# Kernel optimization log

Hardware: AMD Instinct MI355X
Metric: run time of the kernel (lower is better)

## Reference

```python
import jax, jax.numpy as jnp
import numpy as np

N_NODES = 50000


def gcn_layer(x, W, b, src, dst, norm):
    # x: [N, Fin] -> [N, Fout]; PyG GCNConv: x' = D^-1/2 (A+I) D^-1/2 (x W) + b
    h = x @ W
    msg = h[src] * norm[:, None]              # gather + scale per edge (incl. self loops)
    out = jax.ops.segment_sum(msg, dst, num_segments=N_NODES)
    return out + b


def setup_inputs() -> dict:
    key = jax.random.key(0)
    ks = jax.random.split(key, 12)
    F_in, F_hid, T, E = 128, 128, 10, 1600000
    features = jax.random.normal(ks[0], (N_NODES, F_in), dtype=jnp.float32)
    edges = jax.random.randint(ks[1], (2, E), 0, N_NODES, dtype=jnp.int64)
    s = 1.0 / np.sqrt(F_in)
    W0 = jax.random.uniform(ks[2], (F_in, F_hid), jnp.float32, -s, s)
    b0 = jnp.zeros((F_hid,), jnp.float32)
    W1 = jax.random.uniform(ks[3], (F_hid, F_hid), jnp.float32, -s, s)
    b1 = jnp.zeros((F_hid,), jnp.float32)
    W2 = jax.random.uniform(ks[4], (F_hid, F_hid), jnp.float32, -s, s)
    b2 = jnp.zeros((F_hid,), jnp.float32)
    Wout = jax.random.uniform(ks[5], (F_hid, T), jnp.float32, -s, s)
    bout = jax.random.uniform(ks[6], (T,), jnp.float32, -s, s)
    return {"features": features, "edges": edges, "W0": W0, "b0": b0,
            "W1": W1, "b1": b1, "W2": W2, "b2": b2, "Wout": Wout, "bout": bout}


def reference(features, edges, W0, b0, W1, b1, W2, b2, Wout, bout):
    # Add self loops once; edge structure shared across layers.
    loop = jnp.arange(N_NODES, dtype=edges.dtype)
    src = jnp.concatenate([edges[0], loop])
    dst = jnp.concatenate([edges[1], loop])
    deg = jax.ops.segment_sum(jnp.ones_like(dst, dtype=features.dtype), dst,
                              num_segments=N_NODES)
    dinv = jnp.where(deg > 0, jax.lax.rsqrt(deg), 0.0)
    norm = dinv[src] * dinv[dst]              # [E + N]

    x = gcn_layer(features, W0, b0, src, dst, norm)
    x = gcn_layer(x, W1, b1, src, dst, norm)
    x = gcn_layer(x, W2, b2, src, dst, norm)

    pooled = jnp.mean(x, axis=0)              # [F_hid]
    logits = pooled @ Wout + bout             # [T]
    return jax.nn.log_softmax(logits, axis=0).reshape(1, -1)
```

## Files before the change

kernel.cpp:

```cpp
#include <hip/hip_runtime.h>


#define FDIM 128
#define HSZ 12500
#define NBG 64
#define BSZ 196
#define NBKT 256
#define SCB 256
#define STG 6400


__global__ void __launch_bounds__(1024)
k1_count_deg(const int* __restrict__ edges, int E, int e4, int N,
             int* __restrict__ blockCnt, int* __restrict__ partial) {
  __shared__ int h[HSZ];
  __shared__ int cnt[NBKT];
  const int t = threadIdx.x;
  const int bid = blockIdx.x;
  const int g = bid >> 6, j = bid & (NBG - 1);
  const int lo = g * HSZ;
  const int hi = min(N, lo + HSZ);
  const int hs = hi - lo;
  for (int i = t; i < hs; i += 1024) h[i] = 0;
  if (t < NBKT) cnt[t] = 0;
  __syncthreads();

  const int per4 = (e4 + SCB - 1) / SCB;
  const int i0 = bid * per4;
  const int i1 = min(e4, i0 + per4);
  const int4* s4 = (const int4*)edges;
  for (int i = i0 + t; i < i1; i += 1024) {
    int4 s = s4[i];
    atomicAdd(&cnt[s.x / BSZ], 1);
    atomicAdd(&cnt[s.y / BSZ], 1);
    atomicAdd(&cnt[s.z / BSZ], 1);
    atomicAdd(&cnt[s.w / BSZ], 1);
  }
  if (bid == 0) {
    for (int e = 4 * e4 + t; e < E; e += 1024)
      atomicAdd(&cnt[edges[e] / BSZ], 1);
  }

  const int4* d4 = (const int4*)(edges + E);
  for (int i = j * 1024 + t; i < e4; i += NBG * 1024) {
    int4 d = d4[i];
    if (d.x >= lo && d.x < hi) atomicAdd(&h[d.x - lo], 1);
    if (d.y >= lo && d.y < hi) atomicAdd(&h[d.y - lo], 1);
    if (d.z >= lo && d.z < hi) atomicAdd(&h[d.z - lo], 1);
    if (d.w >= lo && d.w < hi) atomicAdd(&h[d.w - lo], 1);
  }
  if (j == 0) {
    const int* dst = edges + E;
    for (int e = 4 * e4 + t; e < E; e += 1024) {
      int d = dst[e];
      if (d >= lo && d < hi) atomicAdd(&h[d - lo], 1);
    }
  }
  __syncthreads();
  if (t < NBKT) blockCnt[bid * NBKT + t] = cnt[t];
  int* op = partial + (size_t)bid * HSZ;
  for (int i = t; i < hs; i += 1024) op[i] = h[i];
}


__global__ void __launch_bounds__(256)
k2_scatter_dinv(const int* __restrict__ edges, int E, int e4, int N,
                const int* __restrict__ blockCnt,
                const int* __restrict__ partial,
                int* __restrict__ bucket, int* __restrict__ meta,
                float* __restrict__ dinv) {
  const int bid = blockIdx.x;
  const int t = threadIdx.x;

  if (bid >= SCB) {
    int n = (bid - SCB) * 256 + t;
    if (n < N) {
      int gg = n / HSZ, off = n - gg * HSZ;
      const int* p = partial + ((size_t)gg * NBG) * HSZ + off;
      int s = 1;
      for (int jj = 0; jj < NBG; ++jj) s += p[(size_t)jj * HSZ];
      dinv[n] = rsqrtf((float)s);
    }
    return;
  }

  __shared__ int baseS[NBKT];
  __shared__ int off2[NBKT];
  __shared__ int offRun[NBKT];
  __shared__ int cntS[NBKT];
  __shared__ int wsum[4];
  __shared__ int stg[STG];

  const int lane = t & 63, wv = t >> 6;
  const int myCnt = blockCnt[bid * NBKT + t];
  int myoff = 0, total = 0;
  for (int b = 0; b < SCB; ++b) {
    int v = blockCnt[b * NBKT + t];
    if (b < bid) myoff += v;
    total += v;
  }
  int inc = total;
  #pragma unroll
  for (int o = 1; o < 64; o <<= 1) {
    int q = __shfl_up(inc, o, 64);
    if (lane >= o) inc += q;
  }
  if (lane == 63) wsum[wv] = inc;
  __syncthreads();
  int wb = 0;
  for (int w = 0; w < wv; ++w) wb += wsum[w];
  const int gbase = wb + inc - total;
  baseS[t] = gbase + myoff;
  if (bid == 0) { meta[t] = gbase; meta[NBKT + t] = total; }
  int inc2 = myCnt;
  #pragma unroll
  for (int o = 1; o < 64; o <<= 1) {
    int q = __shfl_up(inc2, o, 64);
    if (lane >= o) inc2 += q;
  }
  __syncthreads();
  if (lane == 63) wsum[wv] = inc2;
  __syncthreads();
  int wb2 = 0;
  for (int w = 0; w < wv; ++w) wb2 += wsum[w];
  off2[t] = wb2 + inc2 - myCnt;
  offRun[t] = off2[t];
  cntS[t] = myCnt;
  __syncthreads();

  const int per4 = (e4 + SCB - 1) / SCB;
  const int i0 = bid * per4;
  const int i1 = min(e4, i0 + per4);
  const int4* s4 = (const int4*)edges;
  const int4* d4 = (const int4*)(edges + E);
  for (int i = i0 + t; i < i1; i += 256) {
    int4 s = s4[i];
    int4 d = d4[i];
    int b, p;
    b = s.x / BSZ; p = atomicAdd(&offRun[b], 1); stg[p] = ((s.x - b * BSZ) << 16) | d.x;
    b = s.y / BSZ; p = atomicAdd(&offRun[b], 1); stg[p] = ((s.y - b * BSZ) << 16) | d.y;
    b = s.z / BSZ; p = atomicAdd(&offRun[b], 1); stg[p] = ((s.z - b * BSZ) << 16) | d.z;
    b = s.w / BSZ; p = atomicAdd(&offRun[b], 1); stg[p] = ((s.w - b * BSZ) << 16) | d.w;
  }
  if (bid == 0) {
    for (int e = 4 * e4 + t; e < E; e += 256) {
      int s = edges[e], d = edges[E + e];
      int b = s / BSZ;
      int p = atomicAdd(&offRun[b], 1);
      stg[p] = ((s - b * BSZ) << 16) | d;
    }
  }
  __syncthreads();
  for (int k = wv; k < NBKT; k += 4) {
    const int len = cntS[k];
    const int lb = off2[k];
    const int gb = baseS[k];
    for (int i = lane; i < len; i += 64)
      bucket[gb + i] = stg[lb + i];
  }
}


__global__ void __launch_bounds__(1024)
pass_kernel(const int* __restrict__ bucket, const int* __restrict__ meta,
            const float* __restrict__ dinv, const float* __restrict__ win,
            float* __restrict__ wout, float* __restrict__ ssump,
            const float* __restrict__ feat, float* __restrict__ v0p,
            int N, int doV0) {
  __shared__ float uacc[16][200];
  __shared__ float ul[BSZ];
  __shared__ float red[16];
  __shared__ float partS[8][FDIM];
  const int t = threadIdx.x;
  const int wv = t >> 6;
  const int b = blockIdx.x;
  const int n0 = b * BSZ;
  const int ns = min(BSZ, N - n0);

  for (int i = t; i < 16 * 200; i += 1024)
    ((float*)uacc)[i] = 0.f;
  __syncthreads();

  const int base = meta[b];
  const int end = base + meta[NBKT + b];
  for (int i = base + t; i < end; i += 1024) {
    int p = bucket[i];
    atomicAdd(&uacc[wv][p >> 16], win[p & 0xFFFF]);
  }
  __syncthreads();

  float u = 0.f;
  if (t < ns) {
    float s = 0.f;
    #pragma unroll
    for (int k = 0; k < 16; ++k) s += uacc[k][t];
    int n = n0 + t;
    u = dinv[n] * (s + win[n]);
    if (wout) wout[n] = dinv[n] * u;
    ul[t] = u;
  } else if (t < BSZ) {
    ul[t] = 0.f;
  }
  if (ssump) {
    float a = u;
    for (int o = 32; o > 0; o >>= 1) a += __shfl_down(a, o, 64);
    if ((t & 63) == 0) red[wv] = a;
    __syncthreads();
    if (t == 0) {
      float s = 0.f;
      #pragma unroll
      for (int k = 0; k < 16; ++k) s += red[k];
      ssump[b] = s;
    }
  }
  if (doV0) {
    __syncthreads();
    const int f = t & (FDIM - 1);
    const int r8 = t >> 7;
    float acc = 0.f;
    for (int r = r8; r < ns; r += 8)
      acc += ul[r] * feat[(size_t)(n0 + r) * FDIM + f];
    partS[r8][f] = acc;
    __syncthreads();
    if (r8 == 0) {
      float s = 0.f;
      #pragma unroll
      for (int k = 0; k < 8; ++k) s += partS[k][f];
      v0p[(size_t)b * FDIM + f] = s;
    }
  }
}


__global__ void __launch_bounds__(1024)
final_kernel(const float* __restrict__ W0, const float* __restrict__ b0,
             const float* __restrict__ W1, const float* __restrict__ b1,
             const float* __restrict__ W2, const float* __restrict__ b2,
             const float* __restrict__ Wout, const float* __restrict__ bout,
             const float* __restrict__ v0p, int nv0,
             const float* __restrict__ ssumpA,
             const float* __restrict__ ssumpB,
             int nss,
             float* __restrict__ out, int N) {
  __shared__ float Wl[FDIM * FDIM];
  __shared__ float WoL[FDIM * 10];
  __shared__ float va[FDIM], vb[FDIM];
  __shared__ float part[8][FDIM];
  __shared__ float red0[16], red1[16];
  __shared__ float shS1, shS2;
  __shared__ float lg[10];
  const int t = threadIdx.x;
  const int f = t & (FDIM - 1);
  const int sl = t >> 7;

  {
    const float4* w4 = (const float4*)W0;
    float4* l4 = (float4*)Wl;
    #pragma unroll
    for (int i = 0; i < 4; ++i) l4[t + i * 1024] = w4[t + i * 1024];
    if (t < (FDIM * 10) / 4) ((float4*)WoL)[t] = ((const float4*)Wout)[t];
  }
  float acc = 0.f;
  for (int j = sl; j < nv0; j += 8) acc += v0p[(size_t)j * FDIM + f];
  part[sl][f] = acc;
  {
    float a0 = 0.f, a1 = 0.f;
    for (int j = t; j < nss; j += 1024) { a0 += ssumpA[j]; a1 += ssumpB[j]; }
    for (int o = 32; o > 0; o >>= 1) {
      a0 += __shfl_down(a0, o, 64);
      a1 += __shfl_down(a1, o, 64);
    }
    if ((t & 63) == 0) { red0[t >> 6] = a0; red1[t >> 6] = a1; }
  }
  __syncthreads();
  if (sl == 0) {
    float s = 0.f;
    #pragma unroll
    for (int j = 0; j < 8; ++j) s += part[j][f];
    va[f] = s;
  }
  if (t == 0) {
    float x = 0.f, y = 0.f;
    #pragma unroll
    for (int i = 0; i < 16; ++i) { x += red0[i]; y += red1[i]; }
    shS2 = x; shS1 = y;
  }
  __syncthreads();

  acc = 0.f;
  #pragma unroll
  for (int k = 0; k < 16; ++k) {
    int kk = sl * 16 + k;
    acc += va[kk] * Wl[kk * FDIM + f];
  }
  part[sl][f] = acc;
  __syncthreads();
  {
    const float4* w4 = (const float4*)W1;
    float4* l4 = (float4*)Wl;
    #pragma unroll
    for (int i = 0; i < 4; ++i) l4[t + i * 1024] = w4[t + i * 1024];
  }
  if (sl == 0) {
    float s = 0.f;
    #pragma unroll
    for (int j = 0; j < 8; ++j) s += part[j][f];
    vb[f] = s + shS1 * b0[f];
  }
  __syncthreads();

  acc = 0.f;
  #pragma unroll
  for (int k = 0; k < 16; ++k) {
    int kk = sl * 16 + k;
    acc += vb[kk] * Wl[kk * FDIM + f];
  }
  part[sl][f] = acc;
  __syncthreads();
  {
    const float4* w4 = (const float4*)W2;
    float4* l4 = (float4*)Wl;
    #pragma unroll
    for (int i = 0; i < 4; ++i) l4[t + i * 1024] = w4[t + i * 1024];
  }
  if (sl == 0) {
    float s = 0.f;
    #pragma unroll
    for (int j = 0; j < 8; ++j) s += part[j][f];
    va[f] = s + shS2 * b1[f];
  }
  __syncthreads();

  acc = 0.f;
  #pragma unroll
  for (int k = 0; k < 16; ++k) {
    int kk = sl * 16 + k;
    acc += va[kk] * Wl[kk * FDIM + f];
  }
  part[sl][f] = acc;
  __syncthreads();
  if (sl == 0) {
    float s = 0.f;
    #pragma unroll
    for (int j = 0; j < 8; ++j) s += part[j][f];
    vb[f] = s / (float)N + b2[f];
  }
  __syncthreads();

  if (t < 10) {
    float a = 0.f;
    for (int k = 0; k < FDIM; ++k) a += vb[k] * WoL[k * 10 + t];
    lg[t] = a + bout[t];
  }
  __syncthreads();
  if (t == 0) {
    float m = lg[0];
    for (int q = 1; q < 10; ++q) m = fmaxf(m, lg[q]);
    float s = 0.f;
    for (int q = 0; q < 10; ++q) s += expf(lg[q] - m);
    float lse = logf(s);
    for (int q = 0; q < 10; ++q) out[q] = lg[q] - m - lse;
  }
}


__global__ void __launch_bounds__(1024)
hist_deg_kernel(const int* __restrict__ edges, int E, int e4, int N,
                int* __restrict__ partial) {
  __shared__ int h[HSZ];
  const int g = blockIdx.x / NBG;
  const int j = blockIdx.x - g * NBG;
  const int lo = g * HSZ;
  const int hi = min(N, lo + HSZ);
  const int hs = hi - lo;
  for (int i = threadIdx.x; i < hs; i += blockDim.x) h[i] = 0;
  __syncthreads();
  const int* dst = edges + E;
  const int4* dst4 = (const int4*)dst;
  for (int i = j * blockDim.x + threadIdx.x; i < e4; i += NBG * blockDim.x) {
    int4 d = dst4[i];
    if (d.x >= lo && d.x < hi) atomicAdd(&h[d.x - lo], 1);
    if (d.y >= lo && d.y < hi) atomicAdd(&h[d.y - lo], 1);
    if (d.z >= lo && d.z < hi) atomicAdd(&h[d.z - lo], 1);
    if (d.w >= lo && d.w < hi) atomicAdd(&h[d.w - lo], 1);
  }
  if (j == 0) {
    for (int e = 4 * e4 + threadIdx.x; e < E; e += blockDim.x) {
      int d = dst[e];
      if (d >= lo && d < hi) atomicAdd(&h[d - lo], 1);
    }
  }
  __syncthreads();
  int* out = partial + (size_t)blockIdx.x * HSZ;
  for (int i = threadIdx.x; i < hs; i += blockDim.x) out[i] = h[i];
}

__global__ void merge_dinv_kernel(const int* __restrict__ partial,
                                  float* __restrict__ dinv, int N) {
  int n = blockIdx.x * blockDim.x + threadIdx.x;
  if (n >= N) return;
  int g = n / HSZ;
  int off = n - g * HSZ;
  const int* p = partial + ((size_t)g * NBG) * HSZ + off;
  int s = 1;
  for (int jj = 0; jj < NBG; ++jj) s += p[(size_t)jj * HSZ];
  dinv[n] = rsqrtf((float)s);
}

__global__ void __launch_bounds__(1024)
hist_u_kernel(const int* __restrict__ edges, int E, int e4, int N,
              const float* __restrict__ w,
              float* __restrict__ partial) {
  __shared__ float h[HSZ];
  const int g = blockIdx.x / NBG;
  const int j = blockIdx.x - g * NBG;
  const int lo = g * HSZ;
  const int hi = min(N, lo + HSZ);
  const int hs = hi - lo;
  for (int i = threadIdx.x; i < hs; i += blockDim.x) h[i] = 0.f;
  __syncthreads();
  const int4* s4 = (const int4*)edges;
  const int4* d4 = (const int4*)(edges + E);
  for (int i = j * blockDim.x + threadIdx.x; i < e4; i += NBG * blockDim.x) {
    int4 s = s4[i];
    int4 d = d4[i];
    if (s.x >= lo && s.x < hi) atomicAdd(&h[s.x - lo], w[d.x]);
    if (s.y >= lo && s.y < hi) atomicAdd(&h[s.y - lo], w[d.y]);
    if (s.z >= lo && s.z < hi) atomicAdd(&h[s.z - lo], w[d.z]);
    if (s.w >= lo && s.w < hi) atomicAdd(&h[s.w - lo], w[d.w]);
  }
  if (j == 0) {
    const int* se = edges; const int* de = edges + E;
    for (int e = 4 * e4 + threadIdx.x; e < E; e += blockDim.x) {
      int s = se[e], d = de[e];
      if (s >= lo && s < hi) atomicAdd(&h[s - lo], w[d]);
    }
  }
  __syncthreads();
  float* out = partial + (size_t)blockIdx.x * HSZ;
  for (int i = threadIdx.x; i < hs; i += blockDim.x) out[i] = h[i];
}

__global__ void __launch_bounds__(256)
merge_u_kernel(const float* __restrict__ partial,
               const float* __restrict__ dinv,
               const float* __restrict__ win,
               float* __restrict__ uout,
               float* __restrict__ wout,
               float* __restrict__ ssump, int N) {
  __shared__ float red[4];
  int n = blockIdx.x * blockDim.x + threadIdx.x;
  float u = 0.f;
  if (n < N) {
    int g = n / HSZ;
    int off = n - g * HSZ;
    const float* p = partial + ((size_t)g * NBG) * HSZ + off;
    float s = 0.f;
    for (int jj = 0; jj < NBG; ++jj) s += p[(size_t)jj * HSZ];
    u = dinv[n] * (s + win[n]);
    if (uout) uout[n] = u;
    if (wout) wout[n] = dinv[n] * u;
  }
  if (ssump) {
    float a = u;
    for (int o = 32; o > 0; o >>= 1) a += __shfl_down(a, o, 64);
    if ((threadIdx.x & 63) == 0) red[threadIdx.x >> 6] = a;
    __syncthreads();
    if (threadIdx.x == 0)
      ssump[blockIdx.x] = red[0] + red[1] + red[2] + red[3];
  }
}

__global__ void __launch_bounds__(1024)
v0_kernel(const float* __restrict__ feat, const float* __restrict__ u0,
          float* __restrict__ v0p, int N) {
  __shared__ float sh[8][FDIM];
  int f = threadIdx.x & (FDIM - 1);
  int r8 = threadIdx.x >> 7;
  float acc = 0.f;
  for (int r = blockIdx.x * 8 + r8; r < N; r += 128 * 8)
    acc += u0[r] * feat[(size_t)r * FDIM + f];
  sh[r8][f] = acc;
  __syncthreads();
  if (r8 == 0) {
    float s = acc;
    #pragma unroll
    for (int k = 1; k < 8; ++k) s += sh[k][f];
    v0p[(size_t)blockIdx.x * FDIM + f] = s;
  }
}


extern "C" void kernel_launch(void* const* d_in, const int* in_sizes, int n_in,
                              void* d_out, int out_size, void* d_ws, size_t ws_size,
                              hipStream_t stream) {
  const float* feat = (const float*)d_in[0];
  const int*   edges = (const int*)d_in[1];
  const float* W0 = (const float*)d_in[2];
  const float* b0 = (const float*)d_in[3];
  const float* W1 = (const float*)d_in[4];
  const float* b1 = (const float*)d_in[5];
  const float* W2 = (const float*)d_in[6];
  const float* b2 = (const float*)d_in[7];
  const float* Wout = (const float*)d_in[8];
  const float* bout = (const float*)d_in[9];

  const int N = in_sizes[0] / FDIM;
  const int E = in_sizes[1] / 2;
  const int e4 = E >> 2;
  const int mergeGrid = (N + 255) / 256;

  char* ws = (char*)d_ws;
  size_t nb = ((size_t)N * 4 + 511) & ~(size_t)511;
  size_t partB = ((size_t)4 * NBG * HSZ * 4 + 511) & ~(size_t)511;
  size_t v0pB = ((size_t)NBKT * FDIM * 4 + 511) & ~(size_t)511;
  size_t ssBsz = ((size_t)NBKT * 4 + 511) & ~(size_t)511;
  size_t bktB = ((size_t)E * 4 + 511) & ~(size_t)511;
  size_t cntB = (size_t)SCB * NBKT * 4;
  size_t need = partB + 4 * nb + v0pB + 2 * ssBsz + bktB + cntB + 4096;

  char* p = ws;
  float* part = (float*)p;       p += partB;
  float* dinv = (float*)p;       p += nb;
  float* w2   = (float*)p;       p += nb;
  float* w1   = (float*)p;       p += nb;
  float* u0   = (float*)p;       p += nb;
  float* v0p  = (float*)p;       p += v0pB;
  float* ssA  = (float*)p;       p += ssBsz;
  float* ssB_ = (float*)p;       p += ssBsz;
  int* bucket = (int*)p;         p += bktB;
  int* blockCnt = (int*)p;       p += cntB;
  int* meta   = (int*)p;

  const int perBlkEdges = ((e4 + SCB - 1) / SCB) * 4 + 4;
  const bool bucketOK = (ws_size >= need) && (N <= NBKT * BSZ) &&
                        (N <= 65535) && (perBlkEdges <= STG) && ((E & 3) == 0);

  if (bucketOK) {
    k1_count_deg<<<SCB, 1024, 0, stream>>>(edges, E, e4, N,
                                           blockCnt, (int*)part);
    k2_scatter_dinv<<<SCB + mergeGrid, 256, 0, stream>>>(
        edges, E, e4, N, blockCnt, (const int*)part, bucket, meta, dinv);
    pass_kernel<<<NBKT, 1024, 0, stream>>>(bucket, meta, dinv, dinv,
                                           w2, ssA, nullptr, nullptr, N, 0);
    pass_kernel<<<NBKT, 1024, 0, stream>>>(bucket, meta, dinv, w2,
                                           w1, ssB_, nullptr, nullptr, N, 0);
    pass_kernel<<<NBKT, 1024, 0, stream>>>(bucket, meta, dinv, w1,
                                           nullptr, nullptr, feat, v0p, N, 1);
    final_kernel<<<1, 1024, 0, stream>>>(W0, b0, W1, b1, W2, b2, Wout, bout,
                                         v0p, NBKT, ssA, ssB_, NBKT,
                                         (float*)d_out, N);
  } else {
    hist_deg_kernel<<<4 * NBG, 1024, 0, stream>>>(edges, E, e4, N, (int*)part);
    merge_dinv_kernel<<<mergeGrid, 256, 0, stream>>>((const int*)part, dinv, N);
    hist_u_kernel<<<4 * NBG, 1024, 0, stream>>>(edges, E, e4, N, dinv, part);
    merge_u_kernel<<<mergeGrid, 256, 0, stream>>>(part, dinv, dinv,
                                                  nullptr, w2, ssA, N);
    hist_u_kernel<<<4 * NBG, 1024, 0, stream>>>(edges, E, e4, N, w2, part);
    merge_u_kernel<<<mergeGrid, 256, 0, stream>>>(part, dinv, w2,
                                                  nullptr, w1, ssB_, N);
    hist_u_kernel<<<4 * NBG, 1024, 0, stream>>>(edges, E, e4, N, w1, part);
    merge_u_kernel<<<mergeGrid, 256, 0, stream>>>(part, dinv, w1,
                                                  u0, nullptr, nullptr, N);
    v0_kernel<<<128, 1024, 0, stream>>>(feat, u0, v0p, N);
    final_kernel<<<1, 1024, 0, stream>>>(W0, b0, W1, b1, W2, b2, Wout, bout,
                                         v0p, 128, ssA, ssB_, mergeGrid,
                                         (float*)d_out, N);
  }
}
```

Measured before the change: 101.9 us.

## Halve node bucket size to 512 buckets and adapt scatter/scan to two buckets per thread

Doubles the number of destination-node buckets, halving nodes per bucket, so the pass kernel runs twice as many blocks with smaller shared accumulators. This is meant to spread the per-layer aggregation across more CUs. The bucketing kernel's scan now handles two buckets per thread, and the stage-to-global copy now gives each thread a whole bucket to copy serially. That serial copy loses coalescing compared with the previous wave-per-bucket copy, and the larger grid adds per-block overhead.

```diff
diff --git a/kernel.cpp b/kernel.cpp
--- a/kernel.cpp
+++ b/kernel.cpp
@@ -4,8 +4,8 @@
 #define FDIM 128
 #define HSZ 12500
 #define NBG 64
-#define BSZ 196
-#define NBKT 256
+#define BSZ 98
+#define NBKT 512
 #define SCB 256
 #define STG 6400
 
@@ -92,14 +92,18 @@
   __shared__ int stg[STG];
 
   const int lane = t & 63, wv = t >> 6;
-  const int myCnt = blockCnt[bid * NBKT + t];
-  int myoff = 0, total = 0;
+  const int k0 = 2 * t, k1 = 2 * t + 1;
+  const int c0 = blockCnt[bid * NBKT + k0];
+  const int c1 = blockCnt[bid * NBKT + k1];
+  int off0 = 0, off1 = 0, tot0 = 0, tot1 = 0;
   for (int b = 0; b < SCB; ++b) {
-    int v = blockCnt[b * NBKT + t];
-    if (b < bid) myoff += v;
-    total += v;
-  }
-  int inc = total;
+    int v0 = blockCnt[b * NBKT + k0];
+    int v1 = blockCnt[b * NBKT + k1];
+    if (b < bid) { off0 += v0; off1 += v1; }
+    tot0 += v0; tot1 += v1;
+  }
+  int s = tot0 + tot1;
+  int inc = s;
   #pragma unroll
   for (int o = 1; o < 64; o <<= 1) {
     int q = __shfl_up(inc, o, 64);
@@ -109,10 +113,15 @@
   __syncthreads();
   int wb = 0;
   for (int w = 0; w < wv; ++w) wb += wsum[w];
-  const int gbase = wb + inc - total;
-  baseS[t] = gbase + myoff;
-  if (bid == 0) { meta[t] = gbase; meta[NBKT + t] = total; }
-  int inc2 = myCnt;
+  const int ex = wb + inc - s;
+  baseS[k0] = ex + off0;
+  baseS[k1] = ex + tot0 + off1;
+  if (bid == 0) {
+    meta[k0] = ex;            meta[k1] = ex + tot0;
+    meta[NBKT + k0] = tot0;   meta[NBKT + k1] = tot1;
+  }
+  int s2 = c0 + c1;
+  int inc2 = s2;
   #pragma unroll
   for (int o = 1; o < 64; o <<= 1) {
     int q = __shfl_up(inc2, o, 64);
@@ -123,9 +132,10 @@
   __syncthreads();
   int wb2 = 0;
   for (int w = 0; w < wv; ++w) wb2 += wsum[w];
-  off2[t] = wb2 + inc2 - myCnt;
-  offRun[t] = off2[t];
-  cntS[t] = myCnt;
+  const int ex2 = wb2 + inc2 - s2;
+  off2[k0] = ex2;        off2[k1] = ex2 + c0;
+  offRun[k0] = ex2;      offRun[k1] = ex2 + c0;
+  cntS[k0] = c0;         cntS[k1] = c1;
   __syncthreads();
 
   const int per4 = (e4 + SCB - 1) / SCB;
@@ -134,28 +144,28 @@
   const int4* s4 = (const int4*)edges;
   const int4* d4 = (const int4*)(edges + E);
   for (int i = i0 + t; i < i1; i += 256) {
-    int4 s = s4[i];
-    int4 d = d4[i];
+    int4 sv = s4[i];
+    int4 dv = d4[i];
     int b, p;
-    b = s.x / BSZ; p = atomicAdd(&offRun[b], 1); stg[p] = ((s.x - b * BSZ) << 16) | d.x;
-    b = s.y / BSZ; p = atomicAdd(&offRun[b], 1); stg[p] = ((s.y - b * BSZ) << 16) | d.y;
-    b = s.z / BSZ; p = atomicAdd(&offRun[b], 1); stg[p] = ((s.z - b * BSZ) << 16) | d.z;
-    b = s.w / BSZ; p = atomicAdd(&offRun[b], 1); stg[p] = ((s.w - b * BSZ) << 16) | d.w;
+    b = sv.x / BSZ; p = atomicAdd(&offRun[b], 1); stg[p] = ((sv.x - b * BSZ) << 16) | dv.x;
+    b = sv.y / BSZ; p = atomicAdd(&offRun[b], 1); stg[p] = ((sv.y - b * BSZ) << 16) | dv.y;
+    b = sv.z / BSZ; p = atomicAdd(&offRun[b], 1); stg[p] = ((sv.z - b * BSZ) << 16) | dv.z;
+    b = sv.w / BSZ; p = atomicAdd(&offRun[b], 1); stg[p] = ((sv.w - b * BSZ) << 16) | dv.w;
   }
   if (bid == 0) {
     for (int e = 4 * e4 + t; e < E; e += 256) {
-      int s = edges[e], d = edges[E + e];
-      int b = s / BSZ;
+      int sv = edges[e], dv = edges[E + e];
+      int b = sv / BSZ;
       int p = atomicAdd(&offRun[b], 1);
-      stg[p] = ((s - b * BSZ) << 16) | d;
-    }
-  }
-  __syncthreads();
-  for (int k = wv; k < NBKT; k += 4) {
+      stg[p] = ((sv - b * BSZ) << 16) | dv;
+    }
+  }
+  __syncthreads();
+  for (int k = t; k < NBKT; k += 256) {
     const int len = cntS[k];
     const int lb = off2[k];
     const int gb = baseS[k];
-    for (int i = lane; i < len; i += 64)
+    for (int i = 0; i < len; ++i)
       bucket[gb + i] = stg[lb + i];
   }
 }
@@ -167,7 +177,7 @@
             float* __restrict__ wout, float* __restrict__ ssump,
             const float* __restrict__ feat, float* __restrict__ v0p,
             int N, int doV0) {
-  __shared__ float uacc[16][200];
+  __shared__ float uacc[16][100];
   __shared__ float ul[BSZ];
   __shared__ float red[16];
   __shared__ float partS[8][FDIM];
@@ -177,7 +187,7 @@
   const int n0 = b * BSZ;
   const int ns = min(BSZ, N - n0);
 
-  for (int i = t; i < 16 * 200; i += 1024)
+  for (int i = t; i < 16 * 100; i += 1024)
     ((float*)uacc)[i] = 0.f;
   __syncthreads();
 
@@ -517,7 +527,7 @@
   size_t ssBsz = ((size_t)NBKT * 4 + 511) & ~(size_t)511;
   size_t bktB = ((size_t)E * 4 + 511) & ~(size_t)511;
   size_t cntB = (size_t)SCB * NBKT * 4;
-  size_t need = partB + 4 * nb + v0pB + 2 * ssBsz + bktB + cntB + 4096;
+  size_t need = partB + 4 * nb + v0pB + 2 * ssBsz + bktB + cntB + 8192;
 
   char* p = ws;
   float* part = (float*)p;       p += partB;
```

After: 103.6 us. Within noise of the previous version (+1.7%).
